# Kernel optimization log

Measured on AMD Instinct MI355X. Metric: run time of the kernel, lower is better.

The kernel has to match this reference:

```python
import jax, jax.numpy as jnp
import numpy as np

B, T, C, H = 2, 2048, 1024, 16
D = C // H  # 64
RW, RA, RG = 64, 64, 128  # decay / a / gate LoRA ranks
EPS = 1e-5


def setup_inputs() -> dict:
    key = jax.random.key(0)
    ks = iter(jax.random.split(key, 40))
    n = lambda s, sc=0.02: jax.random.normal(next(ks), s, jnp.float32) * sc
    u = lambda s: jax.random.uniform(next(ks), s, jnp.float32)
    return dict(
        hidden_states=jax.random.normal(next(ks), (B, T, C), jnp.float32),
        # token-mix (time-shift lerp) params
        x_r=u((C,)), x_w=u((C,)), x_k=u((C,)), x_v=u((C,)), x_a=u((C,)), x_g=u((C,)),
        k_k=u((C,)), k_a=u((C,)), r_k=n((H, D), 0.1),
        # square projections (stored [in, out]; x @ W)
        W_r=n((C, C)), W_k=n((C, C)), W_v=n((C, C)), W_o=n((C, C)),
        # LoRA: out = act(x @ A) @ Bm + bias (activation between the two linears)
        w_lora_a=n((C, RW)), w_lora_b=n((RW, C)), w_lora_bias=n((C,), 0.1),
        a_lora_a=n((C, RA)), a_lora_b=n((RA, C)), a_lora_bias=jnp.zeros((C,), jnp.float32),
        g_lora_a=n((C, RG)), g_lora_b=n((RG, C)), g_lora_bias=jnp.zeros((C,), jnp.float32),
        # GroupNorm(num_heads groups over value_dim)
        gn_weight=jnp.ones((C,), jnp.float32), gn_bias=jnp.zeros((C,), jnp.float32),
    )


def _rwkv7_scan(r, log_w, k, v, a, b):
    # all inputs [B, T, H, D]; state S: [B, H, D_v, D_k]
    # S_t = S_{t-1} * diag(exp(log_w_t)) + (S_{t-1} @ a_t) b_t^T + v_t k_t^T
    # o_t = S_t @ r_t
    Bn, Tn, Hn, Dn = r.shape

    def step(S, xs):
        r_t, w_t, k_t, v_t, a_t, b_t = xs  # each [B, H, D]
        sa = jnp.einsum('bhij,bhj->bhi', S, a_t)          # S @ a (pre-decay state)
        S = (S * jnp.exp(w_t)[:, :, None, :]
             + sa[..., None] * b_t[:, :, None, :]
             + v_t[..., None] * k_t[:, :, None, :])
        o_t = jnp.einsum('bhij,bhj->bhi', S, r_t)
        return S, o_t

    S0 = jnp.zeros((Bn, Hn, Dn, Dn), r.dtype)
    xs = tuple(jnp.swapaxes(x, 0, 1) for x in (r, log_w, k, v, a, b))  # [T,B,H,D]
    _, o = jax.lax.scan(step, S0, xs)
    return jnp.swapaxes(o, 0, 1)  # [B, T, H, D]


def reference(hidden_states, x_r, x_w, x_k, x_v, x_a, x_g, k_k, k_a, r_k,
              W_r, W_k, W_v, W_o,
              w_lora_a, w_lora_b, w_lora_bias,
              a_lora_a, a_lora_b, a_lora_bias,
              g_lora_a, g_lora_b, g_lora_bias,
              gn_weight, gn_bias):
    Bn, Tn, Cn = hidden_states.shape
    # time shift: pad one step of zeros at the front, drop last
    shifted = jnp.concatenate([jnp.zeros_like(hidden_states[:, :1]), hidden_states[:, :-1]], axis=1)
    delta = shifted - hidden_states

    xr = hidden_states + delta * x_r
    xw = hidden_states + delta * x_w
    xk = hidden_states + delta * x_k
    xv = hidden_states + delta * x_v
    xa = hidden_states + delta * x_a

    r = xr @ W_r
    log_w = -jax.nn.softplus(-((jnp.tanh(xw @ w_lora_a) @ w_lora_b) + w_lora_bias)) - 0.5
    k = xk @ W_k
    v = xv @ W_v
    a = jax.nn.sigmoid((xa @ a_lora_a) @ a_lora_b + a_lora_bias)
    # g_lora(r): sigmoid activation sits BETWEEN the two LoRA linears
    g = jax.nn.sigmoid(r @ g_lora_a) @ g_lora_b + g_lora_bias

    kk = (k * k_k).reshape(Bn, Tn, H, D)
    kk = kk / jnp.maximum(jnp.linalg.norm(kk, axis=-1, keepdims=True), 1e-12)  # per-head L2 norm
    k = k * (1.0 + (a - 1.0) * k_a)

    rh = r.reshape(Bn, Tn, H, D)
    wh = log_w.reshape(Bn, Tn, H, D)
    kh = k.reshape(Bn, Tn, H, D)
    vh = v.reshape(Bn, Tn, H, D)
    ah = a.reshape(Bn, Tn, H, D)

    o = _rwkv7_scan(rh, wh, kh, vh, -kk, kk * ah)  # [B, T, H, D]

    # GroupNorm over value_dim with H groups (stats per head)
    mu = o.mean(-1, keepdims=True)
    var = ((o - mu) ** 2).mean(-1, keepdims=True)
    o_flat = ((o - mu) * jax.lax.rsqrt(var + EPS)).reshape(Bn, Tn, C) * gn_weight + gn_bias

    bonus = ((rh * kh * r_k).sum(-1, keepdims=True) * vh).reshape(Bn, Tn, C)
    o_flat = o_flat + bonus
    return (o_flat * g) @ W_o
```

## Files before the change

### kernel.cpp

```cpp
#include <hip/hip_runtime.h>
#include <hip/hip_bf16.h>
#include <hip/hip_fp16.h>
#include <stdint.h>
#include <stddef.h>

typedef __hip_bfloat16 bf16;
typedef _Float16 f16;
typedef __attribute__((ext_vector_type(8))) short short8;
typedef __attribute__((ext_vector_type(8))) _Float16 half8;
typedef __attribute__((ext_vector_type(4))) float f32x4;
typedef unsigned short us;

__device__ __forceinline__ float dsigm(float z){ return 1.f/(1.f+expf(-z)); }

__device__ __forceinline__ void split1(float v, us& h, us& l) {
  bf16 hb = __float2bfloat16(v);
  h = __builtin_bit_cast(us, hb);
  float hf = __bfloat162float(hb);
  bf16 lb = __float2bfloat16(v - hf);
  l = __builtin_bit_cast(us, lb);
}

__device__ __forceinline__ void split8(const float* f, short8& h, short8& l) {
#pragma unroll
  for (int e = 0; e < 8; ++e) {
    us hh, ll;
    split1(f[e], hh, ll);
    h[e] = (short)hh; l[e] = (short)ll;
  }
}

__device__ __forceinline__ void gl16(const f16* g, f16* l) {
  __builtin_amdgcn_global_load_lds((const __attribute__((address_space(1))) void*)g,
                                   (__attribute__((address_space(3))) void*)l, 16, 0, 0);
}

__device__ __forceinline__ void emit16(const float* __restrict__ marr, int c4,
    const float4& cur, const float4& dlt, f16* __restrict__ out, int row)
{
  float4 m = *(const float4*)(marr + c4);
  f16* o = out + (size_t)row*1024 + c4;
  o[0] = (f16)fmaf(dlt.x, m.x, cur.x);
  o[1] = (f16)fmaf(dlt.y, m.y, cur.y);
  o[2] = (f16)fmaf(dlt.z, m.z, cur.z);
  o[3] = (f16)fmaf(dlt.w, m.w, cur.w);
}

__global__ void k_prep(const float* __restrict__ hs,
    const float* __restrict__ mr, const float* __restrict__ mw, const float* __restrict__ mk,
    const float* __restrict__ mv, const float* __restrict__ ma,
    f16* __restrict__ oxr, f16* __restrict__ oxw, f16* __restrict__ oxk,
    f16* __restrict__ oxv, f16* __restrict__ oxa)
{
  int id = blockIdx.x * 256 + threadIdx.x;
  int row = id >> 8;
  int c4 = (id & 255) << 2;
  int t = row & 2047;
  const float* hp = hs + (size_t)row*1024 + c4;
  float4 cur = *(const float4*)hp;
  float4 prev = make_float4(0.f,0.f,0.f,0.f);
  if (t > 0) prev = *(const float4*)(hp - 1024);
  float4 dlt = make_float4(prev.x-cur.x, prev.y-cur.y, prev.z-cur.z, prev.w-cur.w);
  emit16(mr, c4, cur, dlt, oxr, row);
  emit16(mw, c4, cur, dlt, oxw, row);
  emit16(mk, c4, cur, dlt, oxk, row);
  emit16(mv, c4, cur, dlt, oxv, row);
  emit16(ma, c4, cur, dlt, oxa, row);
}

struct SrcP { const float* p[10]; };
struct DstP { f16* p[10]; };

__global__ void k_transpose(SrcP S, DstP Dd)
{
  static constexpr int TR[10]  = {1024,1024,1024,1024,1024,  64,1024,  64,1024, 128};
  static constexpr int TCC[10] = {1024,1024,1024,1024,  64,1024,  64,1024, 128,1024};
  static constexpr int TCP[10] = {1024,1024,1024,1024, 128,1024, 128,1024, 128,1024};
  int z = blockIdx.z;
  int R = TR[z], Cc = TCC[z], Cp = TCP[z];
  int n0 = blockIdx.x * 32, r0 = blockIdx.y * 32;
  if (n0 >= Cp || r0 >= R) return;
  const float* src = S.p[z];
  f16* dst = Dd.p[z];
  int tx = threadIdx.x, ty = threadIdx.y;
  __shared__ float tile[32][33];
  if (n0 < Cc) {
#pragma unroll
    for (int i = 0; i < 4; ++i)
      tile[ty + 8*i][tx] = src[(size_t)(r0 + ty + 8*i)*Cc + n0 + tx];
    __syncthreads();
#pragma unroll
    for (int i = 0; i < 4; ++i)
      dst[(size_t)(n0 + ty + 8*i)*R + r0 + tx] = (f16)tile[tx][ty + 8*i];
  } else {
#pragma unroll
    for (int i = 0; i < 4; ++i)
      dst[(size_t)(n0 + ty + 8*i)*R + r0 + tx] = (f16)0.f;
  }
}

struct GJob {
  const f16* A;
  const f16* Bt;
  float* C;
  f16* Cpk;
  const float* bias;
  int K; int N; int Npk; int ldc; int act;
  int lda; int ldb;
};
struct GJobs { GJob j[5]; };

__global__ __launch_bounds__(256) void k_gemm_fp16(GJobs jobs)
{
  GJob jb = jobs.j[blockIdx.z];
  const int colBase = blockIdx.y * 128;
  if (colBase >= jb.N) return;
  const int rowBase = blockIdx.x * 128;
  __shared__ __align__(16) f16 As[128*32];
  __shared__ __align__(16) f16 Bs[128*32];
  const int tid = threadIdx.x;
  const int l = tid & 63, w = tid >> 6;
  const int wm = w >> 1, wn = w & 1;
  const int lrow = l & 15, kid = (l >> 4) * 8;
  const int nk = jb.K >> 5;

  const int s0 = w*64 + l, s1 = (4 + w)*64 + l;
  const int ar0 = s0 >> 2, ac0 = (s0 & 3) * 8;
  const int ar1 = s1 >> 2, ac1 = (s1 & 3) * 8;
  const int ld0 = w*512, ld1 = (4 + w)*512;
  const f16* Arow0 = jb.A  + (size_t)(rowBase + ar0)*jb.lda + ac0;
  const f16* Arow1 = jb.A  + (size_t)(rowBase + ar1)*jb.lda + ac1;
  const f16* Brow0 = jb.Bt + (size_t)(colBase + ar0)*jb.ldb + ac0;
  const f16* Brow1 = jb.Bt + (size_t)(colBase + ar1)*jb.ldb + ac1;

  f32x4 acc[4][4];
#pragma unroll
  for (int i = 0; i < 4; ++i)
#pragma unroll
    for (int j = 0; j < 4; ++j) { f32x4 z = {0.f,0.f,0.f,0.f}; acc[i][j] = z; }

  for (int kt = 0; kt < nk; ++kt) {
    const int kh = kt*32;
    gl16(Arow0 + kh, &As[ld0]);  gl16(Arow1 + kh, &As[ld1]);
    gl16(Brow0 + kh, &Bs[ld0]);  gl16(Brow1 + kh, &Bs[ld1]);
    __syncthreads();
    half8 ah[4], bh[4];
#pragma unroll
    for (int mt = 0; mt < 4; ++mt) ah[mt] = *(const half8*)&As[(wm*64 + mt*16 + lrow)*32 + kid];
#pragma unroll
    for (int nt = 0; nt < 4; ++nt) bh[nt] = *(const half8*)&Bs[(wn*64 + nt*16 + lrow)*32 + kid];
#pragma unroll
    for (int mt = 0; mt < 4; ++mt)
#pragma unroll
      for (int nt = 0; nt < 4; ++nt)
        acc[mt][nt] = __builtin_amdgcn_mfma_f32_16x16x32_f16(ah[mt], bh[nt], acc[mt][nt], 0, 0, 0);
    __syncthreads();
  }
#pragma unroll
  for (int mt = 0; mt < 4; ++mt) {
    int row = rowBase + wm*64 + mt*16 + (l >> 4)*4;
#pragma unroll
    for (int nt = 0; nt < 4; ++nt) {
      int col = colBase + wn*64 + nt*16 + (l & 15);
      float bv = (jb.bias != nullptr) ? jb.bias[col] : 0.f;
#pragma unroll
      for (int rg = 0; rg < 4; ++rg) {
        float v = acc[mt][nt][rg] + bv;
        if (jb.act == 1)      v = dsigm(v);
        else if (jb.act == 2) v = tanhf(v);
        else if (jb.act == 3) v = 0.60653066f * dsigm(v);
        if (jb.C) jb.C[(size_t)(row + rg)*jb.ldc + col] = v;
        if (jb.Cpk && col < jb.Npk)
          jb.Cpk[(size_t)(row + rg)*jb.Npk + col] = (f16)v;
      }
    }
  }
}

__global__ void k_scanprep(float* __restrict__ kA, float* __restrict__ aA,
                           const float* __restrict__ kkw, const float* __restrict__ kaw,
                           float* __restrict__ kkA)
{
  size_t gt = (size_t)blockIdx.x * 256u + threadIdx.x;
  int d = (int)(gt & 63);
  size_t flat = gt >> 6;
  int c = (int)((flat & 15) * 64 + d);
  float k0 = kA[gt], av = aA[gt];
  float kkv = k0 * kkw[c];
  float ss = kkv * kkv;
  ss += __shfl_xor(ss, 1);  ss += __shfl_xor(ss, 2);  ss += __shfl_xor(ss, 4);
  ss += __shfl_xor(ss, 8);  ss += __shfl_xor(ss, 16); ss += __shfl_xor(ss, 32);
  float inv = 1.f / fmaxf(sqrtf(ss), 1e-12f);
  float kkn = kkv * inv;
  kkA[gt] = kkn;
  aA[gt]  = kkn * av;
  kA[gt]  = k0 * fmaf(av - 1.f, kaw[c], 1.f);
}

#define SP1_EW 0
#define SP1_KK 256
#define SP1_BB 512
#define SP1_KV 768
#define SP1_RR 1024
#define SP1_VV 1280

__device__ __forceinline__ void step_lds(const float* __restrict__ sb, int s,
    float* u, float* p, float* __restrict__ o0A, float* __restrict__ zA,
    size_t base, int i, int q, int j0)
{
  float4 ew0 = *(const float4*)(sb + SP1_EW + s*64 + j0);
  float4 ew1 = *(const float4*)(sb + SP1_EW + s*64 + j0 + 4);
  float4 kk0 = *(const float4*)(sb + SP1_KK + s*64 + j0);
  float4 kk1 = *(const float4*)(sb + SP1_KK + s*64 + j0 + 4);
  float4 bb0 = *(const float4*)(sb + SP1_BB + s*64 + j0);
  float4 bb1 = *(const float4*)(sb + SP1_BB + s*64 + j0 + 4);
  float4 kv0 = *(const float4*)(sb + SP1_KV + s*64 + j0);
  float4 kv1 = *(const float4*)(sb + SP1_KV + s*64 + j0 + 4);
  float4 rr0 = *(const float4*)(sb + SP1_RR + s*64 + j0);
  float4 rr1 = *(const float4*)(sb + SP1_RR + s*64 + j0 + 4);
  float vi = sb[SP1_VV + s*64 + i];

  float uk = 0.f, pk = 0.f;
#define RED(SI, V, F) { uk += u[SI]*V.F; pk += p[SI]*V.F; }
  RED(0,kk0,x) RED(1,kk0,y) RED(2,kk0,z) RED(3,kk0,w)
  RED(4,kk1,x) RED(5,kk1,y) RED(6,kk1,z) RED(7,kk1,w)
#undef RED
  uk += __shfl_xor(uk, 1); uk += __shfl_xor(uk, 2); uk += __shfl_xor(uk, 4);
  pk += __shfl_xor(pk, 1); pk += __shfl_xor(pk, 2); pk += __shfl_xor(pk, 4);
  const float su = -uk, sp = -pk;
  float oo = 0.f, zz = 0.f;
#define UPD(SI, E, Kv, Bv, Rv, F) { \
    float uu = u[SI]*E.F + su*Bv.F + vi*Kv.F; u[SI] = uu; oo += uu*Rv.F; \
    float pp = p[SI]*E.F + sp*Bv.F;           p[SI] = pp; zz += pp*Rv.F; }
  UPD(0,ew0,kv0,bb0,rr0,x) UPD(1,ew0,kv0,bb0,rr0,y) UPD(2,ew0,kv0,bb0,rr0,z) UPD(3,ew0,kv0,bb0,rr0,w)
  UPD(4,ew1,kv1,bb1,rr1,x) UPD(5,ew1,kv1,bb1,rr1,y) UPD(6,ew1,kv1,bb1,rr1,z) UPD(7,ew1,kv1,bb1,rr1,w)
#undef UPD
  oo += __shfl_xor(oo, 1); oo += __shfl_xor(oo, 2); oo += __shfl_xor(oo, 4);
  zz += __shfl_xor(zz, 1); zz += __shfl_xor(zz, 2); zz += __shfl_xor(zz, 4);
  if (q == 0) { o0A[base + i] = oo; zA[base + i] = zz; }
}

__global__ __launch_bounds__(512) void k_scan_p1(
    const float* __restrict__ rA, const float* __restrict__ ewA,
    const float* __restrict__ kA, const float* __restrict__ vA,
    const float* __restrict__ kkA, const float* __restrict__ bbA,
    float* __restrict__ o0A, float* __restrict__ zA,
    float* __restrict__ UcA, float* __restrict__ PTcA)
{
  const int blk = blockIdx.x;
  const int bh = blk & 31, c = blk >> 5;
  const int b = bh >> 4, h = bh & 15;
  const int tid = threadIdx.x;
  const int i = tid >> 3, q = tid & 7, j0 = q * 8;
  const size_t base0 = (size_t)b*2048*1024 + (size_t)h*64 + (size_t)(c*64)*1024;

  __shared__ __align__(16) float smem[4160];

  const int active = (tid < 384);
  const int a0 = tid >> 6, rm0 = tid & 63, s0 = rm0 >> 4, f40 = rm0 & 15;
  const float* pa0 = (a0==0) ? ewA : (a0==1) ? kkA : (a0==2) ? bbA :
                     (a0==3) ? kA  : (a0==4) ? rA  : vA;
  const float* src0 = pa0 + base0 + (size_t)s0*1024 + f40*4;
  const int dst0 = a0*256 + s0*64 + f40*4;

  float u[8], p[8];
#pragma unroll
  for (int jj = 0; jj < 8; ++jj) { u[jj] = 0.f; p[jj] = (j0 + jj == i) ? 1.f : 0.f; }

  if (active) *(float4*)&smem[dst0] = *(const float4*)(src0);
  __syncthreads();

  int curb = 0;
  for (int g = 0; g < 16; ++g) {
    float4 n0;
    if (g < 15 && active) n0 = *(const float4*)(src0 + (size_t)(g+1)*4096);
    const float* sb = smem + curb*1536;
#pragma unroll
    for (int s = 0; s < 4; ++s)
      step_lds(sb, s, u, p, o0A, zA, base0 + (size_t)(g*4 + s)*1024, i, q, j0);
    if (g < 15 && active) *(float4*)&smem[(curb^1)*1536 + dst0] = n0;
    __syncthreads();
    curb ^= 1;
  }

  const size_t cbase = ((size_t)(bh*32 + c)) * 4096;
  *(float4*)(UcA + cbase + (size_t)i*64 + j0)     = make_float4(u[0],u[1],u[2],u[3]);
  *(float4*)(UcA + cbase + (size_t)i*64 + j0 + 4) = make_float4(u[4],u[5],u[6],u[7]);
  float (*lds)[65] = (float(*)[65])smem;
#pragma unroll
  for (int jj = 0; jj < 8; ++jj) lds[i][j0 + jj] = p[jj];
  __syncthreads();
  float4 w0 = make_float4(lds[j0+0][i], lds[j0+1][i], lds[j0+2][i], lds[j0+3][i]);
  float4 w1 = make_float4(lds[j0+4][i], lds[j0+5][i], lds[j0+6][i], lds[j0+7][i]);
  *(float4*)(PTcA + cbase + (size_t)i*64 + j0)     = w0;
  *(float4*)(PTcA + cbase + (size_t)i*64 + j0 + 4) = w1;
}

__device__ __forceinline__ void chain_body(int c, int bh, int w, int lr, int lq,
    float (&Slds)[64][65], f32x4 (&acc)[4],
    float (&u_c)[4][4], float4 (&p_c)[2][2],
    float (&u_n)[4][4], float4 (&p_n)[2][2],
    const float* __restrict__ UcA, const float* __restrict__ PTcA,
    float* __restrict__ S0A)
{
  const size_t s0base = ((size_t)bh*32 + c) * 4096;
#pragma unroll
  for (int mt = 0; mt < 4; ++mt)
#pragma unroll
    for (int rg = 0; rg < 4; ++rg) {
      Slds[mt*16 + lq*4 + rg][w*16 + lr] = acc[mt][rg];
      if (c > 0) S0A[s0base + (size_t)(mt*16 + lq*4 + rg)*64 + w*16 + lr] = acc[mt][rg];
    }
  __syncthreads();
  if (c + 1 < 32) {
    const size_t nbase = ((size_t)bh*32 + c + 1) * 4096;
#pragma unroll
    for (int mt = 0; mt < 4; ++mt)
#pragma unroll
      for (int rg = 0; rg < 4; ++rg)
        u_n[mt][rg] = UcA[nbase + (size_t)(mt*16 + lq*4 + rg)*64 + w*16 + lr];
#pragma unroll
    for (int kt = 0; kt < 2; ++kt)
#pragma unroll
      for (int hh = 0; hh < 2; ++hh)
        p_n[kt][hh] = *(const float4*)(PTcA + nbase + (size_t)(w*16 + lr)*64 + kt*32 + lq*8 + hh*4);
  }
  short8 pbh[2], pbl[2];
#pragma unroll
  for (int kt = 0; kt < 2; ++kt) {
    float f[8] = {p_c[kt][0].x, p_c[kt][0].y, p_c[kt][0].z, p_c[kt][0].w,
                  p_c[kt][1].x, p_c[kt][1].y, p_c[kt][1].z, p_c[kt][1].w};
    split8(f, pbh[kt], pbl[kt]);
  }
  f32x4 nacc[4];
#pragma unroll
  for (int mt = 0; mt < 4; ++mt) {
    f32x4 z = {u_c[mt][0], u_c[mt][1], u_c[mt][2], u_c[mt][3]};
    nacc[mt] = z;
  }
#pragma unroll
  for (int kt = 0; kt < 2; ++kt)
#pragma unroll
    for (int mt = 0; mt < 4; ++mt) {
      float f[8];
#pragma unroll
      for (int e = 0; e < 8; ++e) f[e] = Slds[mt*16 + lr][kt*32 + lq*8 + e];
      short8 sah, sal;
      split8(f, sah, sal);
      nacc[mt] = __builtin_amdgcn_mfma_f32_16x16x32_bf16(sah, pbh[kt], nacc[mt], 0, 0, 0);
      nacc[mt] = __builtin_amdgcn_mfma_f32_16x16x32_bf16(sal, pbh[kt], nacc[mt], 0, 0, 0);
      nacc[mt] = __builtin_amdgcn_mfma_f32_16x16x32_bf16(sah, pbl[kt], nacc[mt], 0, 0, 0);
    }
#pragma unroll
  for (int mt = 0; mt < 4; ++mt) acc[mt] = nacc[mt];
  __syncthreads();
}

__global__ __launch_bounds__(256) void k_chain(
    const float* __restrict__ UcA, const float* __restrict__ PTcA,
    float* __restrict__ S0A)
{
  const int bh = blockIdx.x;
  const int l = threadIdx.x & 63, w = threadIdx.x >> 6;
  const int lr = l & 15, lq = l >> 4;
  __shared__ float Slds[64][65];

  f32x4 acc[4];
#pragma unroll
  for (int mt = 0; mt < 4; ++mt) { f32x4 z = {0.f,0.f,0.f,0.f}; acc[mt] = z; }

  float u0[4][4], u1[4][4];
  float4 p0[2][2], p1[2][2];
  {
    const size_t cbase = (size_t)bh * 32 * 4096;
#pragma unroll
    for (int mt = 0; mt < 4; ++mt)
#pragma unroll
      for (int rg = 0; rg < 4; ++rg)
        u0[mt][rg] = UcA[cbase + (size_t)(mt*16 + lq*4 + rg)*64 + w*16 + lr];
#pragma unroll
    for (int kt = 0; kt < 2; ++kt)
#pragma unroll
      for (int hh = 0; hh < 2; ++hh)
        p0[kt][hh] = *(const float4*)(PTcA + cbase + (size_t)(w*16 + lr)*64 + kt*32 + lq*8 + hh*4);
  }
  for (int c = 0; c < 32; c += 2) {
    chain_body(c,     bh, w, lr, lq, Slds, acc, u0, p0, u1, p1, UcA, PTcA, S0A);
    chain_body(c + 1, bh, w, lr, lq, Slds, acc, u1, p1, u0, p0, UcA, PTcA, S0A);
  }
}

__global__ __launch_bounds__(256) void k_corrpost(
    const float* __restrict__ S0A, const float* __restrict__ zA,
    const float* __restrict__ o0A, const float* __restrict__ rA,
    const float* __restrict__ kA, const float* __restrict__ vA,
    const float* __restrict__ rk, const float* __restrict__ gnw,
    const float* __restrict__ gnb, const float* __restrict__ gA,
    f16* __restrict__ yH)
{
  const int blk = blockIdx.x;
  const int bh = blk & 31;
  const int c  = blk >> 5;
  const int b = bh >> 4, h = bh & 15;
  const int l = threadIdx.x & 63, w = threadIdx.x >> 6;
  const int lr = l & 15, lq = l >> 4;

  f32x4 a2[4];
#pragma unroll
  for (int nt = 0; nt < 4; ++nt) { f32x4 z = {0.f,0.f,0.f,0.f}; a2[nt] = z; }

  if (c > 0) {
    const size_t s0base = ((size_t)bh*32 + c) * 4096;
    short8 sbh[4][2], sbl[4][2];
#pragma unroll
    for (int nt = 0; nt < 4; ++nt)
#pragma unroll
      for (int kt = 0; kt < 2; ++kt) {
        float f[8];
#pragma unroll
        for (int e = 0; e < 8; ++e)
          f[e] = S0A[s0base + (size_t)(nt*16 + lr)*64 + kt*32 + lq*8 + e];
        split8(f, sbh[nt][kt], sbl[nt][kt]);
      }
    short8 zh[2], zl[2];
#pragma unroll
    for (int kt = 0; kt < 2; ++kt) {
      const float* zp = zA + ((size_t)(b*2048 + c*64 + w*16 + lr)*16 + h)*64 + kt*32 + lq*8;
      float f[8];
#pragma unroll
      for (int e = 0; e < 8; ++e) f[e] = zp[e];
      split8(f, zh[kt], zl[kt]);
    }
#pragma unroll
    for (int kt = 0; kt < 2; ++kt)
#pragma unroll
      for (int nt = 0; nt < 4; ++nt) {
        a2[nt] = __builtin_amdgcn_mfma_f32_16x16x32_bf16(zh[kt], sbh[nt][kt], a2[nt], 0, 0, 0);
        a2[nt] = __builtin_amdgcn_mfma_f32_16x16x32_bf16(zl[kt], sbh[nt][kt], a2[nt], 0, 0, 0);
        a2[nt] = __builtin_amdgcn_mfma_f32_16x16x32_bf16(zh[kt], sbl[nt][kt], a2[nt], 0, 0, 0);
      }
  }

#pragma unroll
  for (int rg = 0; rg < 4; ++rg) {
    const int tl = w*16 + lq*4 + rg;
    const size_t trow = (size_t)(b*2048 + c*64 + tl);
    const size_t rb = trow*1024 + h*64;
    float o4[4], v4[4];
    float sum = 0.f, pr = 0.f;
#pragma unroll
    for (int nt = 0; nt < 4; ++nt) {
      const int ii = nt*16 + lr;
      float o = o0A[rb + ii] + a2[nt][rg];
      o4[nt] = o; sum += o;
      v4[nt] = vA[rb + ii];
      pr += rA[rb + ii] * kA[rb + ii] * rk[h*64 + ii];
    }
    sum += __shfl_xor(sum,1); sum += __shfl_xor(sum,2);
    sum += __shfl_xor(sum,4); sum += __shfl_xor(sum,8);
    pr  += __shfl_xor(pr,1);  pr  += __shfl_xor(pr,2);
    pr  += __shfl_xor(pr,4);  pr  += __shfl_xor(pr,8);
    float mean = sum * (1.f/64.f);
    float vp = 0.f;
#pragma unroll
    for (int nt = 0; nt < 4; ++nt) { float d = o4[nt]-mean; vp += d*d; }
    vp += __shfl_xor(vp,1); vp += __shfl_xor(vp,2);
    vp += __shfl_xor(vp,4); vp += __shfl_xor(vp,8);
    float inv = rsqrtf(vp*(1.f/64.f) + 1e-5f);
#pragma unroll
    for (int nt = 0; nt < 4; ++nt) {
      const int ii = nt*16 + lr;
      const int ch = h*64 + ii;
      float y = (o4[nt]-mean)*inv*gnw[ch] + gnb[ch];
      y = fmaf(pr, v4[nt], y);
      y *= gA[rb + ii];
      yH[trow*1024 + ch] = (f16)y;
    }
  }
}

extern "C" void kernel_launch(void* const* d_in, const int* in_sizes, int n_in,
                              void* d_out, int out_size, void* d_ws, size_t ws_size,
                              hipStream_t stream)
{
  (void)in_sizes; (void)n_in; (void)out_size; (void)ws_size;
  const float* hs     = (const float*)d_in[0];
  const float* x_r    = (const float*)d_in[1];
  const float* x_w    = (const float*)d_in[2];
  const float* x_k    = (const float*)d_in[3];
  const float* x_v    = (const float*)d_in[4];
  const float* x_a    = (const float*)d_in[5];
  const float* k_k    = (const float*)d_in[7];
  const float* k_a    = (const float*)d_in[8];
  const float* r_k    = (const float*)d_in[9];
  const float* W_r    = (const float*)d_in[10];
  const float* W_k    = (const float*)d_in[11];
  const float* W_v    = (const float*)d_in[12];
  const float* W_o    = (const float*)d_in[13];
  const float* wla    = (const float*)d_in[14];
  const float* wlb    = (const float*)d_in[15];
  const float* wlbias = (const float*)d_in[16];
  const float* ala    = (const float*)d_in[17];
  const float* alb    = (const float*)d_in[18];
  const float* albias = (const float*)d_in[19];
  const float* gla    = (const float*)d_in[20];
  const float* glb    = (const float*)d_in[21];
  const float* glbias = (const float*)d_in[22];
  const float* gnw    = (const float*)d_in[23];
  const float* gnb    = (const float*)d_in[24];

  char* ws = (char*)d_ws;
  size_t cur = 0;
  auto take = [&](size_t bytes) { size_t o = cur; cur += (bytes + 255) & ~(size_t)255; return o; };

  f16* xr_h = (f16*)(ws + take((size_t)4096*1024*2));
  f16* xw_h = (f16*)(ws + take((size_t)4096*1024*2));
  f16* xk_h = (f16*)(ws + take((size_t)4096*1024*2));
  f16* xv_h = (f16*)(ws + take((size_t)4096*1024*2));
  f16* xa_h = (f16*)(ws + take((size_t)4096*1024*2));
  f16* Wr_p  = (f16*)(ws + take((size_t)1024*1024*2));
  f16* Wk_p  = (f16*)(ws + take((size_t)1024*1024*2));
  f16* Wv_p  = (f16*)(ws + take((size_t)1024*1024*2));
  f16* Wo_p  = (f16*)(ws + take((size_t)1024*1024*2));
  f16* wla_p = (f16*)(ws + take((size_t)128*1024*2));
  f16* wlb_p = (f16*)(ws + take((size_t)1024*64*2));
  f16* ala_p = (f16*)(ws + take((size_t)128*1024*2));
  f16* alb_p = (f16*)(ws + take((size_t)1024*64*2));
  f16* gla_p = (f16*)(ws + take((size_t)128*1024*2));
  f16* glb_p = (f16*)(ws + take((size_t)1024*128*2));
  f16* r_h  = (f16*)(ws + take((size_t)4096*1024*2));
  f16* t2w  = (f16*)(ws + take((size_t)4096*64*2));
  f16* t2a  = (f16*)(ws + take((size_t)4096*64*2));
  f16* t2g  = (f16*)(ws + take((size_t)4096*128*2));
  float* r_f  = (float*)(ws + take((size_t)4096*1024*4));
  float* k_f  = (float*)(ws + take((size_t)4096*1024*4));
  float* v_f  = (float*)(ws + take((size_t)4096*1024*4));
  float* kk_f = (float*)(ws + take((size_t)4096*1024*4));
  float* z_f  = (float*)(ws + take((size_t)4096*1024*4));
  float* Uc_f = (float*)(ws + take((size_t)4096*1024*4));
  float* PT_f = (float*)(ws + take((size_t)4096*1024*4));
  float* ew_f = (float*)xr_h;
  float* a_f  = (float*)xk_h;
  float* g_f  = (float*)xa_h;
  g_f = (float*)(ws + take((size_t)4096*1024*4));
  float* S0_f = kk_f;
  f16*   y_h  = (f16*)xr_h;
  float* oF   = (float*)d_out;

  k_prep<<<4096, 256, 0, stream>>>(hs, x_r, x_w, x_k, x_v, x_a,
                                   xr_h, xw_h, xk_h, xv_h, xa_h);
  SrcP sp; DstP dp;
  sp.p[0]=W_r; sp.p[1]=W_k; sp.p[2]=W_v; sp.p[3]=W_o;
  sp.p[4]=wla; sp.p[5]=wlb; sp.p[6]=ala; sp.p[7]=alb; sp.p[8]=gla; sp.p[9]=glb;
  dp.p[0]=Wr_p; dp.p[1]=Wk_p; dp.p[2]=Wv_p; dp.p[3]=Wo_p;
  dp.p[4]=wla_p; dp.p[5]=wlb_p; dp.p[6]=ala_p; dp.p[7]=alb_p; dp.p[8]=gla_p; dp.p[9]=glb_p;
  k_transpose<<<dim3(32,32,10), dim3(32,8), 0, stream>>>(sp, dp);

  GJobs J{};
  auto job = [](const f16* A, const f16* Bt, float* C, f16* Cpk, const float* bias,
                int K, int N, int Npk, int ldc, int act, int lda, int ldb) {
    GJob j; j.A=A; j.Bt=Bt; j.C=C; j.Cpk=Cpk; j.bias=bias;
    j.K=K; j.N=N; j.Npk=Npk; j.ldc=ldc; j.act=act; j.lda=lda; j.ldb=ldb;
    return j;
  };

  J.j[0] = job(xr_h, Wr_p,  r_f, r_h,     nullptr, 1024, 1024, 1024, 1024, 0, 1024, 1024);
  J.j[1] = job(xk_h, Wk_p,  k_f, nullptr, nullptr, 1024, 1024, 0,    1024, 0, 1024, 1024);
  J.j[2] = job(xv_h, Wv_p,  v_f, nullptr, nullptr, 1024, 1024, 0,    1024, 0, 1024, 1024);
  J.j[3] = job(xw_h, wla_p, nullptr, t2w, nullptr, 1024, 128,  64,   0,    2, 1024, 1024);
  J.j[4] = job(xa_h, ala_p, nullptr, t2a, nullptr, 1024, 128,  64,   0,    0, 1024, 1024);
  k_gemm_fp16<<<dim3(32,8,5), 256, 0, stream>>>(J);

  J = GJobs{};
  J.j[0] = job(t2w, wlb_p, ew_f, nullptr, wlbias, 64,   1024, 0,   1024, 3, 64,   64);
  J.j[1] = job(t2a, alb_p, a_f,  nullptr, albias, 64,   1024, 0,   1024, 1, 64,   64);
  J.j[2] = job(r_h, gla_p, nullptr, t2g,  nullptr, 1024, 128, 128,  0,    1, 1024, 1024);
  k_gemm_fp16<<<dim3(32,8,3), 256, 0, stream>>>(J);

  J = GJobs{};
  J.j[0] = job(t2g, glb_p, g_f, nullptr, glbias, 128, 1024, 0, 1024, 0, 128, 128);
  k_gemm_fp16<<<dim3(32,8,1), 256, 0, stream>>>(J);

  k_scanprep<<<16384, 256, 0, stream>>>(k_f, a_f, k_k, k_a, kk_f);

  k_scan_p1<<<1024, 512, 0, stream>>>(r_f, ew_f, k_f, v_f, kk_f, a_f, oF, z_f, Uc_f, PT_f);
  k_chain<<<32, 256, 0, stream>>>(Uc_f, PT_f, S0_f);

  k_corrpost<<<1024, 256, 0, stream>>>(S0_f, z_f, oF, r_f, k_f, v_f,
                                       r_k, gnw, gnb, g_f, y_h);

  J = GJobs{};
  J.j[0] = job(y_h, Wo_p, (float*)d_out, nullptr, nullptr, 1024, 1024, 0, 1024, 0, 1024, 1024);
  k_gemm_fp16<<<dim3(32,8,1), 256, 0, stream>>>(J);
}
```

Before: 391.8 us.

## Store scan intermediates in fp16 to halve memory traffic across pipeline

The GEMM epilogues now write r, k, v, decay, a and g as fp16 instead of fp32. The scan-prep, chunked scan and post-processing kernels are changed to read and write fp16 and to widen values to fp32 for the arithmetic. Scan-prep is vectorised to 8 elements per thread, and the scan's LDS staging now loads 8 timesteps per group instead of 4. This cuts global and LDS bandwidth for the memory-bound middle stages, at the cost of lower precision in the scan inputs, notably the decay factors, which could hurt accuracy over long sequences.

```diff
diff --git a/kernel.cpp b/kernel.cpp
--- a/kernel.cpp
+++ b/kernel.cpp
@@ -177,73 +177,73 @@
   }
 }
 
-__global__ void k_scanprep(float* __restrict__ kA, float* __restrict__ aA,
+__global__ void k_scanprep(f16* __restrict__ kA, f16* __restrict__ aA,
                            const float* __restrict__ kkw, const float* __restrict__ kaw,
-                           float* __restrict__ kkA)
-{
-  size_t gt = (size_t)blockIdx.x * 256u + threadIdx.x;
-  int d = (int)(gt & 63);
-  size_t flat = gt >> 6;
-  int c = (int)((flat & 15) * 64 + d);
-  float k0 = kA[gt], av = aA[gt];
-  float kkv = k0 * kkw[c];
-  float ss = kkv * kkv;
-  ss += __shfl_xor(ss, 1);  ss += __shfl_xor(ss, 2);  ss += __shfl_xor(ss, 4);
-  ss += __shfl_xor(ss, 8);  ss += __shfl_xor(ss, 16); ss += __shfl_xor(ss, 32);
+                           f16* __restrict__ kkA)
+{
+  int idx = blockIdx.x * 256 + threadIdx.x;
+  size_t gt8 = (size_t)idx * 8;
+  int ch = (int)(gt8 & 1023);
+  half8 k8 = *(const half8*)(kA + gt8);
+  half8 a8 = *(const half8*)(aA + gt8);
+  float kw[8], ka_[8];
+  *(float4*)&kw[0]  = *(const float4*)(kkw + ch);
+  *(float4*)&kw[4]  = *(const float4*)(kkw + ch + 4);
+  *(float4*)&ka_[0] = *(const float4*)(kaw + ch);
+  *(float4*)&ka_[4] = *(const float4*)(kaw + ch + 4);
+  float kkv[8]; float ss = 0.f;
+#pragma unroll
+  for (int e = 0; e < 8; ++e) { kkv[e] = (float)k8[e] * kw[e]; ss += kkv[e]*kkv[e]; }
+  ss += __shfl_xor(ss, 1); ss += __shfl_xor(ss, 2); ss += __shfl_xor(ss, 4);
   float inv = 1.f / fmaxf(sqrtf(ss), 1e-12f);
-  float kkn = kkv * inv;
-  kkA[gt] = kkn;
-  aA[gt]  = kkn * av;
-  kA[gt]  = k0 * fmaf(av - 1.f, kaw[c], 1.f);
-}
-
-#define SP1_EW 0
-#define SP1_KK 256
-#define SP1_BB 512
-#define SP1_KV 768
-#define SP1_RR 1024
-#define SP1_VV 1280
-
-__device__ __forceinline__ void step_lds(const float* __restrict__ sb, int s,
+  half8 kkn8, bb8, kup8;
+#pragma unroll
+  for (int e = 0; e < 8; ++e) {
+    float kkn = kkv[e] * inv;
+    float av = (float)a8[e];
+    kkn8[e] = (f16)kkn;
+    bb8[e]  = (f16)(kkn * av);
+    kup8[e] = (f16)((float)k8[e] * fmaf(av - 1.f, ka_[e], 1.f));
+  }
+  *(half8*)(kkA + gt8) = kkn8;
+  *(half8*)(aA + gt8)  = bb8;
+  *(half8*)(kA + gt8)  = kup8;
+}
+
+__device__ __forceinline__ void step_lds(const f16* __restrict__ sb, int s,
     float* u, float* p, float* __restrict__ o0A, float* __restrict__ zA,
     size_t base, int i, int q, int j0)
 {
-  float4 ew0 = *(const float4*)(sb + SP1_EW + s*64 + j0);
-  float4 ew1 = *(const float4*)(sb + SP1_EW + s*64 + j0 + 4);
-  float4 kk0 = *(const float4*)(sb + SP1_KK + s*64 + j0);
-  float4 kk1 = *(const float4*)(sb + SP1_KK + s*64 + j0 + 4);
-  float4 bb0 = *(const float4*)(sb + SP1_BB + s*64 + j0);
-  float4 bb1 = *(const float4*)(sb + SP1_BB + s*64 + j0 + 4);
-  float4 kv0 = *(const float4*)(sb + SP1_KV + s*64 + j0);
-  float4 kv1 = *(const float4*)(sb + SP1_KV + s*64 + j0 + 4);
-  float4 rr0 = *(const float4*)(sb + SP1_RR + s*64 + j0);
-  float4 rr1 = *(const float4*)(sb + SP1_RR + s*64 + j0 + 4);
-  float vi = sb[SP1_VV + s*64 + i];
+  half8 ew = *(const half8*)(sb + 0    + s*64 + j0);
+  half8 kk = *(const half8*)(sb + 512  + s*64 + j0);
+  half8 bb = *(const half8*)(sb + 1024 + s*64 + j0);
+  half8 kv = *(const half8*)(sb + 1536 + s*64 + j0);
+  half8 rr = *(const half8*)(sb + 2048 + s*64 + j0);
+  float vi = (float)sb[2560 + s*64 + i];
 
   float uk = 0.f, pk = 0.f;
-#define RED(SI, V, F) { uk += u[SI]*V.F; pk += p[SI]*V.F; }
-  RED(0,kk0,x) RED(1,kk0,y) RED(2,kk0,z) RED(3,kk0,w)
-  RED(4,kk1,x) RED(5,kk1,y) RED(6,kk1,z) RED(7,kk1,w)
-#undef RED
+#pragma unroll
+  for (int e = 0; e < 8; ++e) { uk += u[e]*(float)kk[e]; pk += p[e]*(float)kk[e]; }
   uk += __shfl_xor(uk, 1); uk += __shfl_xor(uk, 2); uk += __shfl_xor(uk, 4);
   pk += __shfl_xor(pk, 1); pk += __shfl_xor(pk, 2); pk += __shfl_xor(pk, 4);
   const float su = -uk, sp = -pk;
   float oo = 0.f, zz = 0.f;
-#define UPD(SI, E, Kv, Bv, Rv, F) { \
-    float uu = u[SI]*E.F + su*Bv.F + vi*Kv.F; u[SI] = uu; oo += uu*Rv.F; \
-    float pp = p[SI]*E.F + sp*Bv.F;           p[SI] = pp; zz += pp*Rv.F; }
-  UPD(0,ew0,kv0,bb0,rr0,x) UPD(1,ew0,kv0,bb0,rr0,y) UPD(2,ew0,kv0,bb0,rr0,z) UPD(3,ew0,kv0,bb0,rr0,w)
-  UPD(4,ew1,kv1,bb1,rr1,x) UPD(5,ew1,kv1,bb1,rr1,y) UPD(6,ew1,kv1,bb1,rr1,z) UPD(7,ew1,kv1,bb1,rr1,w)
-#undef UPD
+#pragma unroll
+  for (int e = 0; e < 8; ++e) {
+    float uu = u[e]*(float)ew[e] + su*(float)bb[e] + vi*(float)kv[e];
+    u[e] = uu; oo += uu*(float)rr[e];
+    float pp = p[e]*(float)ew[e] + sp*(float)bb[e];
+    p[e] = pp; zz += pp*(float)rr[e];
+  }
   oo += __shfl_xor(oo, 1); oo += __shfl_xor(oo, 2); oo += __shfl_xor(oo, 4);
   zz += __shfl_xor(zz, 1); zz += __shfl_xor(zz, 2); zz += __shfl_xor(zz, 4);
   if (q == 0) { o0A[base + i] = oo; zA[base + i] = zz; }
 }
 
 __global__ __launch_bounds__(512) void k_scan_p1(
-    const float* __restrict__ rA, const float* __restrict__ ewA,
-    const float* __restrict__ kA, const float* __restrict__ vA,
-    const float* __restrict__ kkA, const float* __restrict__ bbA,
+    const f16* __restrict__ rA, const f16* __restrict__ ewA,
+    const f16* __restrict__ kA, const f16* __restrict__ vA,
+    const f16* __restrict__ kkA, const f16* __restrict__ bbA,
     float* __restrict__ o0A, float* __restrict__ zA,
     float* __restrict__ UcA, float* __restrict__ PTcA)
 {
@@ -255,30 +255,31 @@
   const size_t base0 = (size_t)b*2048*1024 + (size_t)h*64 + (size_t)(c*64)*1024;
 
   __shared__ __align__(16) float smem[4160];
+  f16* hsm = (f16*)smem;
 
   const int active = (tid < 384);
-  const int a0 = tid >> 6, rm0 = tid & 63, s0 = rm0 >> 4, f40 = rm0 & 15;
-  const float* pa0 = (a0==0) ? ewA : (a0==1) ? kkA : (a0==2) ? bbA :
-                     (a0==3) ? kA  : (a0==4) ? rA  : vA;
-  const float* src0 = pa0 + base0 + (size_t)s0*1024 + f40*4;
-  const int dst0 = a0*256 + s0*64 + f40*4;
+  const int a0 = tid >> 6, rm0 = tid & 63, s0 = rm0 >> 3, f0 = rm0 & 7;
+  const f16* pa0 = (a0==0) ? ewA : (a0==1) ? kkA : (a0==2) ? bbA :
+                   (a0==3) ? kA  : (a0==4) ? rA  : vA;
+  const f16* src0 = pa0 + base0 + (size_t)s0*1024 + f0*8;
+  const int dst0 = a0*512 + s0*64 + f0*8;
 
   float u[8], p[8];
 #pragma unroll
   for (int jj = 0; jj < 8; ++jj) { u[jj] = 0.f; p[jj] = (j0 + jj == i) ? 1.f : 0.f; }
 
-  if (active) *(float4*)&smem[dst0] = *(const float4*)(src0);
+  if (active) *(half8*)&hsm[dst0] = *(const half8*)(src0);
   __syncthreads();
 
   int curb = 0;
-  for (int g = 0; g < 16; ++g) {
-    float4 n0;
-    if (g < 15 && active) n0 = *(const float4*)(src0 + (size_t)(g+1)*4096);
-    const float* sb = smem + curb*1536;
-#pragma unroll
-    for (int s = 0; s < 4; ++s)
-      step_lds(sb, s, u, p, o0A, zA, base0 + (size_t)(g*4 + s)*1024, i, q, j0);
-    if (g < 15 && active) *(float4*)&smem[(curb^1)*1536 + dst0] = n0;
+  for (int g = 0; g < 8; ++g) {
+    half8 n0;
+    if (g < 7 && active) n0 = *(const half8*)(src0 + (size_t)(g+1)*8192);
+    const f16* sb = hsm + curb*3072;
+#pragma unroll
+    for (int s = 0; s < 8; ++s)
+      step_lds(sb, s, u, p, o0A, zA, base0 + (size_t)(g*8 + s)*1024, i, q, j0);
+    if (g < 7 && active) *(half8*)&hsm[(curb^1)*3072 + dst0] = n0;
     __syncthreads();
     curb ^= 1;
   }
@@ -392,10 +393,10 @@
 
 __global__ __launch_bounds__(256) void k_corrpost(
     const float* __restrict__ S0A, const float* __restrict__ zA,
-    const float* __restrict__ o0A, const float* __restrict__ rA,
-    const float* __restrict__ kA, const float* __restrict__ vA,
+    const float* __restrict__ o0A, const f16* __restrict__ rA,
+    const f16* __restrict__ kA, const f16* __restrict__ vA,
     const float* __restrict__ rk, const float* __restrict__ gnw,
-    const float* __restrict__ gnb, const float* __restrict__ gA,
+    const float* __restrict__ gnb, const f16* __restrict__ gA,
     f16* __restrict__ yH)
 {
   const int blk = blockIdx.x;
@@ -453,8 +454,8 @@
       const int ii = nt*16 + lr;
       float o = o0A[rb + ii] + a2[nt][rg];
       o4[nt] = o; sum += o;
-      v4[nt] = vA[rb + ii];
-      pr += rA[rb + ii] * kA[rb + ii] * rk[h*64 + ii];
+      v4[nt] = (float)vA[rb + ii];
+      pr += (float)rA[rb + ii] * (float)kA[rb + ii] * rk[h*64 + ii];
     }
     sum += __shfl_xor(sum,1); sum += __shfl_xor(sum,2);
     sum += __shfl_xor(sum,4); sum += __shfl_xor(sum,8);
@@ -473,7 +474,7 @@
       const int ch = h*64 + ii;
       float y = (o4[nt]-mean)*inv*gnw[ch] + gnb[ch];
       y = fmaf(pr, v4[nt], y);
-      y *= gA[rb + ii];
+      y *= (float)gA[rb + ii];
       yH[trow*1024 + ch] = (f16)y;
     }
   }
@@ -529,22 +530,20 @@
   f16* gla_p = (f16*)(ws + take((size_t)128*1024*2));
   f16* glb_p = (f16*)(ws + take((size_t)1024*128*2));
   f16* r_h  = (f16*)(ws + take((size_t)4096*1024*2));
+  f16* k_h  = (f16*)(ws + take((size_t)4096*1024*2));
+  f16* v_h  = (f16*)(ws + take((size_t)4096*1024*2));
+  f16* kk_h = (f16*)(ws + take((size_t)4096*1024*2));
+  f16* g_h  = (f16*)(ws + take((size_t)4096*1024*2));
   f16* t2w  = (f16*)(ws + take((size_t)4096*64*2));
   f16* t2a  = (f16*)(ws + take((size_t)4096*64*2));
   f16* t2g  = (f16*)(ws + take((size_t)4096*128*2));
-  float* r_f  = (float*)(ws + take((size_t)4096*1024*4));
-  float* k_f  = (float*)(ws + take((size_t)4096*1024*4));
-  float* v_f  = (float*)(ws + take((size_t)4096*1024*4));
-  float* kk_f = (float*)(ws + take((size_t)4096*1024*4));
   float* z_f  = (float*)(ws + take((size_t)4096*1024*4));
   float* Uc_f = (float*)(ws + take((size_t)4096*1024*4));
   float* PT_f = (float*)(ws + take((size_t)4096*1024*4));
-  float* ew_f = (float*)xr_h;
-  float* a_f  = (float*)xk_h;
-  float* g_f  = (float*)xa_h;
-  g_f = (float*)(ws + take((size_t)4096*1024*4));
-  float* S0_f = kk_f;
-  f16*   y_h  = (f16*)xr_h;
+  f16*   ew_h = xw_h;
+  f16*   a_h  = xa_h;
+  f16*   y_h  = xr_h;
+  float* S0_f = (float*)xk_h;
   float* oF   = (float*)d_out;
 
   k_prep<<<4096, 256, 0, stream>>>(hs, x_r, x_w, x_k, x_v, x_a,
@@ -564,30 +563,30 @@
     return j;
   };
 
-  J.j[0] = job(xr_h, Wr_p,  r_f, r_h,     nullptr, 1024, 1024, 1024, 1024, 0, 1024, 1024);
-  J.j[1] = job(xk_h, Wk_p,  k_f, nullptr, nullptr, 1024, 1024, 0,    1024, 0, 1024, 1024);
-  J.j[2] = job(xv_h, Wv_p,  v_f, nullptr, nullptr, 1024, 1024, 0,    1024, 0, 1024, 1024);
-  J.j[3] = job(xw_h, wla_p, nullptr, t2w, nullptr, 1024, 128,  64,   0,    2, 1024, 1024);
-  J.j[4] = job(xa_h, ala_p, nullptr, t2a, nullptr, 1024, 128,  64,   0,    0, 1024, 1024);
+  J.j[0] = job(xr_h, Wr_p,  nullptr, r_h, nullptr, 1024, 1024, 1024, 0, 0, 1024, 1024);
+  J.j[1] = job(xk_h, Wk_p,  nullptr, k_h, nullptr, 1024, 1024, 1024, 0, 0, 1024, 1024);
+  J.j[2] = job(xv_h, Wv_p,  nullptr, v_h, nullptr, 1024, 1024, 1024, 0, 0, 1024, 1024);
+  J.j[3] = job(xw_h, wla_p, nullptr, t2w, nullptr, 1024, 128,  64,   0, 2, 1024, 1024);
+  J.j[4] = job(xa_h, ala_p, nullptr, t2a, nullptr, 1024, 128,  64,   0, 0, 1024, 1024);
   k_gemm_fp16<<<dim3(32,8,5), 256, 0, stream>>>(J);
 
   J = GJobs{};
-  J.j[0] = job(t2w, wlb_p, ew_f, nullptr, wlbias, 64,   1024, 0,   1024, 3, 64,   64);
-  J.j[1] = job(t2a, alb_p, a_f,  nullptr, albias, 64,   1024, 0,   1024, 1, 64,   64);
-  J.j[2] = job(r_h, gla_p, nullptr, t2g,  nullptr, 1024, 128, 128,  0,    1, 1024, 1024);
+  J.j[0] = job(t2w, wlb_p, nullptr, ew_h, wlbias, 64,   1024, 1024, 0, 3, 64,   64);
+  J.j[1] = job(t2a, alb_p, nullptr, a_h,  albias, 64,   1024, 1024, 0, 1, 64,   64);
+  J.j[2] = job(r_h, gla_p, nullptr, t2g,  nullptr, 1024, 128,  128,  0, 1, 1024, 1024);
   k_gemm_fp16<<<dim3(32,8,3), 256, 0, stream>>>(J);
 
   J = GJobs{};
-  J.j[0] = job(t2g, glb_p, g_f, nullptr, glbias, 128, 1024, 0, 1024, 0, 128, 128);
+  J.j[0] = job(t2g, glb_p, nullptr, g_h, glbias, 128, 1024, 1024, 0, 0, 128, 128);
   k_gemm_fp16<<<dim3(32,8,1), 256, 0, stream>>>(J);
 
-  k_scanprep<<<16384, 256, 0, stream>>>(k_f, a_f, k_k, k_a, kk_f);
-
-  k_scan_p1<<<1024, 512, 0, stream>>>(r_f, ew_f, k_f, v_f, kk_f, a_f, oF, z_f, Uc_f, PT_f);
+  k_scanprep<<<2048, 256, 0, stream>>>(k_h, a_h, k_k, k_a, kk_h);
+
+  k_scan_p1<<<1024, 512, 0, stream>>>(r_h, ew_h, k_h, v_h, kk_h, a_h, oF, z_f, Uc_f, PT_f);
   k_chain<<<32, 256, 0, stream>>>(Uc_f, PT_f, S0_f);
 
-  k_corrpost<<<1024, 256, 0, stream>>>(S0_f, z_f, oF, r_f, k_f, v_f,
-                                       r_k, gnw, gnb, g_f, y_h);
+  k_corrpost<<<1024, 256, 0, stream>>>(S0_f, z_f, oF, r_h, k_h, v_h,
+                                       r_k, gnw, gnb, g_h, y_h);
 
   J = GJobs{};
   J.j[0] = job(y_h, Wo_p, (float*)d_out, nullptr, nullptr, 1024, 1024, 0, 1024, 0, 1024, 1024);
```

New measurement: 368.5 us. 6.0% less time.
